# Kernel optimization log

Hardware: AMD Instinct MI355X
Metric: run time of the kernel (lower is better)

The kernel has to match this reference:

```python
import jax, jax.numpy as jnp
import numpy as np

D = 1024  # input_size == hidden_size
T = 8192  # decoder sequence length


def setup_inputs() -> dict:
    key = jax.random.key(0)
    ks = jax.random.split(key, 12)
    s = 1.0 / np.sqrt(2 * D)  # nn.Linear default init scale
    return {
        "target_seq": jax.random.normal(ks[0], (T, D), dtype=jnp.float32),
        "encoder_h": jax.random.normal(ks[1], (D,), dtype=jnp.float32),
        "encoder_c": jax.random.normal(ks[2], (D,), dtype=jnp.float32),
        "W_f": jax.random.normal(ks[3], (D, 2 * D), dtype=jnp.float32) * s,
        "b_f": jax.random.normal(ks[4], (D,), dtype=jnp.float32) * 0.1,
        "W_i": jax.random.normal(ks[5], (D, 2 * D), dtype=jnp.float32) * s,
        "b_i": jax.random.normal(ks[6], (D,), dtype=jnp.float32) * 0.1,
        "W_C": jax.random.normal(ks[7], (D, 2 * D), dtype=jnp.float32) * s,
        "b_C": jax.random.normal(ks[8], (D,), dtype=jnp.float32) * 0.1,
        "W_o": jax.random.normal(ks[9], (D, 2 * D), dtype=jnp.float32) * s,
        "b_o": jax.random.normal(ks[10], (D,), dtype=jnp.float32) * 0.1,
        "tf": 0,
    }


def reference(target_seq, encoder_h, encoder_c, W_f, b_f, W_i, b_i, W_C, b_C, W_o, b_o, tf):
    # tf_ratio is hard-coded 0.0 in the source, so teacher forcing never fires.
    def step(carry, x_t):
        h, c = carry
        z_hx = jnp.concatenate([h, x_t])   # cat([h_{t-1}, x_t])
        z_hc = jnp.concatenate([h, c])     # quirk: Ctilde gets cat([h_{t-1}, c_{t-1}])
        f = jax.nn.sigmoid(W_f @ z_hx + b_f)
        i = jax.nn.sigmoid(W_i @ z_hx + b_i)
        ctilde = jnp.tanh(W_C @ z_hc + b_C)
        c_new = f * c + i * ctilde
        o = jax.nn.sigmoid(W_o @ z_hx + b_o)
        h_new = o * jnp.tanh(c_new)
        return (h_new, c_new), h_new

    (_, _), predictions = jax.lax.scan(step, (encoder_h, encoder_c), target_seq)
    return predictions  # [T, D]
```

## Files before the change

kernel.cpp:

```cpp
#include <hip/hip_runtime.h>

#define DD 1024
#define TT 8192
#define NBLK 128
#define NTHR 512
#define RPB 8
#define WLDS (RPB * 4 * DD)
#define LDSB ((WLDS + 4 * DD) * 4)

typedef unsigned long long u64;

__device__ __forceinline__ float fast_sigmoid(float x) {
  x = fminf(fmaxf(x, -30.0f), 30.0f);
  return 1.0f / (1.0f + __expf(-x));
}

__device__ __forceinline__ float fast_tanh(float x) {
  x = fminf(fmaxf(x, -15.0f), 15.0f);
  float e = __expf(2.0f * x);
  return (e - 1.0f) / (e + 1.0f);
}

union HC { u64 u; float2 f; };

__global__ __launch_bounds__(NTHR, 1) void lstm_seq(
    const float* __restrict__ X,
    const float* __restrict__ enc_h,
    const float* __restrict__ enc_c,
    const float* __restrict__ Wf, const float* __restrict__ bf_,
    const float* __restrict__ Wi, const float* __restrict__ bi_,
    const float* __restrict__ Wc, const float* __restrict__ bc_,
    const float* __restrict__ Wo, const float* __restrict__ bo_,
    float* __restrict__ out,
    u64* __restrict__ hcbuf,
    unsigned* __restrict__ flags)
{
  extern __shared__ float lds[];
  const int wv   = threadIdx.x >> 6;
  const int lane = threadIdx.x & 63;
  const int j    = blockIdx.x * RPB + wv;

  for (int idx = threadIdx.x; idx < RPB * 4 * 256; idx += NTHR) {
    const int r = idx >> 10, g = (idx >> 8) & 3, q = idx & 255;
    const int row = blockIdx.x * RPB + r;
    const float* ws = (g == 0) ? Wf : (g == 1) ? Wi : (g == 2) ? Wo : Wc;
    *(float4*)&lds[idx * 4] = *(const float4*)(ws + (size_t)row * 2048 + q * 4);
  }

  float wxf[16], wxi[16], wxo[16], wcc[16];
#pragma unroll
  for (int kb = 0; kb < 4; ++kb) {
    const int k = 1024 + kb * 256 + lane * 4;
    *(float4*)&wxf[kb*4] = *(const float4*)(Wf + (size_t)j * 2048 + k);
    *(float4*)&wxi[kb*4] = *(const float4*)(Wi + (size_t)j * 2048 + k);
    *(float4*)&wxo[kb*4] = *(const float4*)(Wo + (size_t)j * 2048 + k);
    *(float4*)&wcc[kb*4] = *(const float4*)(Wc + (size_t)j * 2048 + k);
  }
  const float Bf = bf_[j], Bi = bi_[j], Bc = bc_[j], Bo = bo_[j];
  const float* lw = lds + wv * 4096;
  float* hst = lds + WLDS;
  float* cst = lds + WLDS + 2 * DD;

  float cj = enc_c[j];

  __syncthreads();

  float4 xc0, xc1, xc2, xc3;
  {
    const float* xq = X + lane * 4;
    xc0 = *(const float4*)(xq);       xc1 = *(const float4*)(xq + 256);
    xc2 = *(const float4*)(xq + 512); xc3 = *(const float4*)(xq + 768);
  }

  for (int t = 0; t < TT; ++t) {
    float4 xn0, xn1, xn2, xn3;
    {
      const size_t tn = (t + 1 < TT) ? (size_t)(t + 1) : (size_t)t;
      const float* xq = X + tn * DD + lane * 4;
      xn0 = *(const float4*)(xq);       xn1 = *(const float4*)(xq + 256);
      xn2 = *(const float4*)(xq + 512); xn3 = *(const float4*)(xq + 768);
    }

    float aF = 0.0f, aI = 0.0f, aO = 0.0f, aC = 0.0f;
#pragma unroll
    for (int kb = 0; kb < 4; ++kb) {
      const float4 xv = (kb==0)?xc0:(kb==1)?xc1:(kb==2)?xc2:xc3;
      const int b = kb * 4;
      aF += wxf[b]*xv.x + wxf[b+1]*xv.y + wxf[b+2]*xv.z + wxf[b+3]*xv.w;
      aI += wxi[b]*xv.x + wxi[b+1]*xv.y + wxi[b+2]*xv.z + wxi[b+3]*xv.w;
      aO += wxo[b]*xv.x + wxo[b+1]*xv.y + wxo[b+2]*xv.z + wxo[b+3]*xv.w;
    }

    const int rp = (t - 1) & 1;

    if (t > 0) {
      if (wv == 0) {
        const unsigned tt = (unsigned)t;
        for (;;) {
          unsigned a = __hip_atomic_load(&flags[lane     ], __ATOMIC_RELAXED, __HIP_MEMORY_SCOPE_AGENT);
          unsigned b = __hip_atomic_load(&flags[lane + 64], __ATOMIC_RELAXED, __HIP_MEMORY_SCOPE_AGENT);
          if (__all((a >= tt) & (b >= tt))) break;
        }
        const u64* src = hcbuf + (size_t)rp * DD + lane;
        u64 raw[16];
#pragma unroll
        for (int q = 0; q < 16; ++q) raw[q] = __hip_atomic_load(src + q * 64,
                                        __ATOMIC_RELAXED, __HIP_MEMORY_SCOPE_AGENT);
#pragma unroll
        for (int q = 0; q < 16; ++q) {
          HC u; u.u = raw[q];
          hst[rp * DD + q * 64 + lane] = u.f.x;
          cst[rp * DD + q * 64 + lane] = u.f.y;
        }
      }
      __syncthreads();

#pragma unroll
      for (int kb = 0; kb < 4; ++kb) {
        const int o = kb * 256 + lane * 4;
        const float4 hv = *(const float4*)&hst[rp * DD + o];
        const float4 cc = *(const float4*)&cst[rp * DD + o];
        const float4 wF = *(const float4*)&lw[o];
        const float4 wI = *(const float4*)&lw[1024 + o];
        const float4 wO = *(const float4*)&lw[2048 + o];
        const float4 wC = *(const float4*)&lw[3072 + o];
        const int b = kb * 4;
        aF += wF.x*hv.x + wF.y*hv.y + wF.z*hv.z + wF.w*hv.w;
        aI += wI.x*hv.x + wI.y*hv.y + wI.z*hv.z + wI.w*hv.w;
        aO += wO.x*hv.x + wO.y*hv.y + wO.z*hv.z + wO.w*hv.w;
        aC += wC.x*hv.x + wC.y*hv.y + wC.z*hv.z + wC.w*hv.w;
        aC += wcc[b]*cc.x + wcc[b+1]*cc.y + wcc[b+2]*cc.z + wcc[b+3]*cc.w;
      }
    } else {
      const float* hp = enc_h + lane * 4;
      const float* cp = enc_c + lane * 4;
#pragma unroll
      for (int kb = 0; kb < 4; ++kb) {
        const int o = kb * 256 + lane * 4;
        const float4 hv = *(const float4*)(hp + kb * 256);
        const float4 cc = *(const float4*)(cp + kb * 256);
        const float4 wF = *(const float4*)&lw[o];
        const float4 wI = *(const float4*)&lw[1024 + o];
        const float4 wO = *(const float4*)&lw[2048 + o];
        const float4 wC = *(const float4*)&lw[3072 + o];
        const int b = kb * 4;
        aF += wF.x*hv.x + wF.y*hv.y + wF.z*hv.z + wF.w*hv.w;
        aI += wI.x*hv.x + wI.y*hv.y + wI.z*hv.z + wI.w*hv.w;
        aO += wO.x*hv.x + wO.y*hv.y + wO.z*hv.z + wO.w*hv.w;
        aC += wC.x*hv.x + wC.y*hv.y + wC.z*hv.z + wC.w*hv.w;
        aC += wcc[b]*cc.x + wcc[b+1]*cc.y + wcc[b+2]*cc.z + wcc[b+3]*cc.w;
      }
    }

#pragma unroll
    for (int m = 32; m >= 1; m >>= 1) {
      aF += __shfl_xor(aF, m, 64);
      aI += __shfl_xor(aI, m, 64);
      aO += __shfl_xor(aO, m, 64);
      aC += __shfl_xor(aC, m, 64);
    }

    const float fg = fast_sigmoid(aF + Bf);
    const float ig = fast_sigmoid(aI + Bi);
    const float og = fast_sigmoid(aO + Bo);
    const float ct = fast_tanh(aC + Bc);
    const float cn = fg * cj + ig * ct;
    const float hn = og * fast_tanh(cn);
    cj = cn;

    if (lane == 0) {
      out[(size_t)t * DD + j] = hn;
      HC u; u.f = make_float2(hn, cn);
      __hip_atomic_store(hcbuf + (size_t)(t & 1) * DD + j, u.u,
                         __ATOMIC_RELAXED, __HIP_MEMORY_SCOPE_AGENT);
    }
    __syncthreads();
    if (threadIdx.x == 0) {
      __hip_atomic_store(&flags[blockIdx.x], (unsigned)(t + 1),
                         __ATOMIC_RELAXED, __HIP_MEMORY_SCOPE_AGENT);
    }
    xc0 = xn0; xc1 = xn1; xc2 = xn2; xc3 = xn3;
  }
}

extern "C" void kernel_launch(void* const* d_in, const int* in_sizes, int n_in,
                              void* d_out, int out_size, void* d_ws, size_t ws_size,
                              hipStream_t stream) {
  const float* X    = (const float*)d_in[0];
  const float* eh   = (const float*)d_in[1];
  const float* ec   = (const float*)d_in[2];
  const float* Wf   = (const float*)d_in[3];
  const float* bf_  = (const float*)d_in[4];
  const float* Wi   = (const float*)d_in[5];
  const float* bi_  = (const float*)d_in[6];
  const float* Wc   = (const float*)d_in[7];
  const float* bc_  = (const float*)d_in[8];
  const float* Wo   = (const float*)d_in[9];
  const float* bo_  = (const float*)d_in[10];
  float* out = (float*)d_out;

  unsigned* flags = (unsigned*)d_ws;
  u64* hcbuf = (u64*)((char*)d_ws + 1024);

  hipMemsetAsync(d_ws, 0, 1024, stream);

  hipFuncSetAttribute((const void*)lstm_seq,
                      hipFuncAttributeMaxDynamicSharedMemorySize, LDSB);

  void* args[] = {(void*)&X, (void*)&eh, (void*)&ec,
                  (void*)&Wf, (void*)&bf_, (void*)&Wi, (void*)&bi_,
                  (void*)&Wc, (void*)&bc_, (void*)&Wo, (void*)&bo_,
                  (void*)&out, (void*)&hcbuf, (void*)&flags};
  hipError_t e = hipLaunchCooperativeKernel((const void*)lstm_seq,
                                            dim3(NBLK), dim3(NTHR),
                                            args, LDSB, stream);
  if (e != hipSuccess) {
    lstm_seq<<<dim3(NBLK), dim3(NTHR), LDSB, stream>>>(
        X, eh, ec, Wf, bf_, Wi, bi_, Wc, bc_, Wo, bo_, out, hcbuf, flags);
  }
}
```

Before: 24.14 ms.

## Embed step tags in packed h/c words to skip flag polling round-trip

Each published h/c word now carries a 16-bit step tag in the top bits, and c is stored as bf16 to make room. Consumers read the h/c buffer directly and accept it when every tag matches the current step. They fall back to polling the flags only when some entries are stale, removing one global-memory round-trip per timestep on the critical path. The cost is lower precision for c in the C-tilde input. The tag also wraps at 65536, which is safe here only because T=8192.

```diff
diff --git a/kernel.cpp b/kernel.cpp
--- a/kernel.cpp
+++ b/kernel.cpp
@@ -21,7 +21,9 @@
   return (e - 1.0f) / (e + 1.0f);
 }
 
-union HC { u64 u; float2 f; };
+__device__ __forceinline__ u64 ld_cp(const u64* p) {
+  return __hip_atomic_load(p, __ATOMIC_RELAXED, __HIP_MEMORY_SCOPE_AGENT);
+}
 
 __global__ __launch_bounds__(NTHR, 1) void lstm_seq(
     const float* __restrict__ X,
@@ -32,7 +34,7 @@
     const float* __restrict__ Wc, const float* __restrict__ bc_,
     const float* __restrict__ Wo, const float* __restrict__ bo_,
     float* __restrict__ out,
-    u64* __restrict__ hcbuf,
+    u64* __restrict__ hcw,
     unsigned* __restrict__ flags)
 {
   extern __shared__ float lds[];
@@ -71,6 +73,8 @@
     xc0 = *(const float4*)(xq);       xc1 = *(const float4*)(xq + 256);
     xc2 = *(const float4*)(xq + 512); xc3 = *(const float4*)(xq + 768);
   }
+
+  const int rot = blockIdx.x & 15;
 
   for (int t = 0; t < TT; ++t) {
     float4 xn0, xn1, xn2, xn3;
@@ -95,22 +99,35 @@
 
     if (t > 0) {
       if (wv == 0) {
-        const unsigned tt = (unsigned)t;
-        for (;;) {
-          unsigned a = __hip_atomic_load(&flags[lane     ], __ATOMIC_RELAXED, __HIP_MEMORY_SCOPE_AGENT);
-          unsigned b = __hip_atomic_load(&flags[lane + 64], __ATOMIC_RELAXED, __HIP_MEMORY_SCOPE_AGENT);
-          if (__all((a >= tt) & (b >= tt))) break;
+        const unsigned want = (unsigned)t;
+        const u64* src = hcw + (size_t)rp * DD + lane;
+        u64 raw[16];
+#pragma unroll
+        for (int q = 0; q < 16; ++q) {
+          const int qr = (q + rot) & 15;
+          raw[qr] = ld_cp(src + qr * 64);
         }
-        const u64* src = hcbuf + (size_t)rp * DD + lane;
-        u64 raw[16];
-#pragma unroll
-        for (int q = 0; q < 16; ++q) raw[q] = __hip_atomic_load(src + q * 64,
-                                        __ATOMIC_RELAXED, __HIP_MEMORY_SCOPE_AGENT);
+        bool ok = true;
+#pragma unroll
+        for (int q = 0; q < 16; ++q) ok &= ((unsigned)(raw[q] >> 48) == want);
+        if (!__all(ok)) {
+          const u64* fl = (const u64*)flags;
+          for (;;) {
+            u64 f = __hip_atomic_load(&fl[lane], __ATOMIC_RELAXED,
+                                      __HIP_MEMORY_SCOPE_AGENT);
+            if (__all(((unsigned)f >= want) & ((unsigned)(f >> 32) >= want)))
+              break;
+          }
+#pragma unroll
+          for (int q = 0; q < 16; ++q) {
+            if ((unsigned)(raw[q] >> 48) != want) raw[q] = ld_cp(src + q * 64);
+          }
+        }
 #pragma unroll
         for (int q = 0; q < 16; ++q) {
-          HC u; u.u = raw[q];
-          hst[rp * DD + q * 64 + lane] = u.f.x;
-          cst[rp * DD + q * 64 + lane] = u.f.y;
+          hst[rp * DD + q * 64 + lane] = __uint_as_float((unsigned)raw[q]);
+          cst[rp * DD + q * 64 + lane] =
+              __uint_as_float(((unsigned)(raw[q] >> 32) & 0xFFFFu) << 16);
         }
       }
       __syncthreads();
@@ -170,8 +187,12 @@
 
     if (lane == 0) {
       out[(size_t)t * DD + j] = hn;
-      HC u; u.f = make_float2(hn, cn);
-      __hip_atomic_store(hcbuf + (size_t)(t & 1) * DD + j, u.u,
+      const unsigned hb = __float_as_uint(hn);
+      const unsigned cb = __float_as_uint(cn);
+      const unsigned cbf = (cb + 0x7FFFu + ((cb >> 16) & 1u)) >> 16;
+      const u64 w = ((u64)(unsigned)(t + 1) << 48) |
+                    ((u64)(cbf & 0xFFFFu) << 32) | (u64)hb;
+      __hip_atomic_store(&hcw[(size_t)(t & 1) * DD + j], w,
                          __ATOMIC_RELAXED, __HIP_MEMORY_SCOPE_AGENT);
     }
     __syncthreads();
@@ -200,9 +221,9 @@
   float* out = (float*)d_out;
 
   unsigned* flags = (unsigned*)d_ws;
-  u64* hcbuf = (u64*)((char*)d_ws + 1024);
-
-  hipMemsetAsync(d_ws, 0, 1024, stream);
+  u64* hcw = (u64*)((char*)d_ws + 1024);
+
+  hipMemsetAsync(d_ws, 0, 1024 + 16384, stream);
 
   hipFuncSetAttribute((const void*)lstm_seq,
                       hipFuncAttributeMaxDynamicSharedMemorySize, LDSB);
@@ -210,12 +231,12 @@
   void* args[] = {(void*)&X, (void*)&eh, (void*)&ec,
                   (void*)&Wf, (void*)&bf_, (void*)&Wi, (void*)&bi_,
                   (void*)&Wc, (void*)&bc_, (void*)&Wo, (void*)&bo_,
-                  (void*)&out, (void*)&hcbuf, (void*)&flags};
+                  (void*)&out, (void*)&hcw, (void*)&flags};
   hipError_t e = hipLaunchCooperativeKernel((const void*)lstm_seq,
                                             dim3(NBLK), dim3(NTHR),
                                             args, LDSB, stream);
   if (e != hipSuccess) {
     lstm_seq<<<dim3(NBLK), dim3(NTHR), LDSB, stream>>>(
-        X, eh, ec, Wf, bf_, Wi, bi_, Wc, bc_, Wo, bo_, out, hcbuf, flags);
-  }
-}
+        X, eh, ec, Wf, bf_, Wi, bi_, Wc, bc_, Wo, bo_, out, hcw, flags);
+  }
+}
```

After: 42.84 ms. +77.5%, slower.
